# Kernel optimization log

Measured on AMD Instinct MI355X. Metric: run time of the kernel, lower is better.

## Reference

```python
import jax, jax.numpy as jnp
import numpy as np

N_NODES = 50000
N_EDGES = 312500
IN_F = 256
OUT_F = 256


def setup_inputs() -> dict:
    key = jax.random.key(0)
    kx, ki, kj, kw, kb = jax.random.split(key, 5)
    x = jax.random.normal(kx, (N_NODES, IN_F), dtype=jnp.float32)
    Ai = jax.random.randint(ki, (N_EDGES,), 0, N_NODES, dtype=jnp.int64)
    Aj = jax.random.randint(kj, (N_EDGES,), 0, N_NODES, dtype=jnp.int64)
    # Linear(2*in_features, out_features): PyTorch default uniform(-1/sqrt(fan_in), 1/sqrt(fan_in))
    bound = 1.0 / np.sqrt(2 * IN_F)
    W = jax.random.uniform(kw, (OUT_F, 2 * IN_F), dtype=jnp.float32, minval=-bound, maxval=bound)
    b = jax.random.uniform(kb, (OUT_F,), dtype=jnp.float32, minval=-bound, maxval=bound)
    return {"x": x, "W": W, "b": b, "Ai": Ai, "Aj": Aj}


def reference(x, W, b, Ai, Aj):
    X_i = x[Ai]                      # [E, F] gather source rows
    X_j = x[Aj]                      # [E, F]
    X_ij = jnp.concatenate([X_i, X_j], axis=1)   # [E, 2F]
    E_msg = jnp.einsum('ef,of->eo', X_ij, W) + b  # [E, out]
    agg_xi = jax.ops.segment_sum(E_msg, Ai, num_segments=N_NODES)  # [N, out]
    return agg_xi
```

## Files before the change

kernel.cpp:

```cpp
#include <hip/hip_runtime.h>
#include <hip/hip_bf16.h>

#define NN 50000
#define NE 312500
#define FIN 256
#define NT 1564
#define CAP 64

typedef __attribute__((ext_vector_type(4))) float f32x4;
typedef __attribute__((ext_vector_type(2))) float f32x2;
typedef __attribute__((ext_vector_type(8))) short bf16x8;
typedef __attribute__((ext_vector_type(4))) unsigned short u16x4;
typedef __attribute__((ext_vector_type(8))) unsigned short u16x8;
typedef __attribute__((ext_vector_type(4))) unsigned int u32x4;

#ifndef __has_builtin
#define __has_builtin(x) 0
#endif
#if __has_builtin(__builtin_amdgcn_cvt_pk_f32_fp8) && __has_builtin(__builtin_amdgcn_cvt_pk_fp8_f32)
#define HWFP8 1
#else
#define HWFP8 0
#endif

__device__ __forceinline__ float bf2f(unsigned short u) {
  return __builtin_bit_cast(float, ((unsigned int)u) << 16);
}
__device__ __forceinline__ unsigned short f2bf(float f) {
  return __builtin_bit_cast(unsigned short, __float2bfloat16(f));
}

#if !HWFP8
__device__ __forceinline__ unsigned enc8(float f) {
  unsigned bits = __builtin_bit_cast(unsigned, f);
  unsigned s = bits >> 31;
  unsigned a = bits & 0x7FFFFFFFu;
  if (a < 0x3C400000u) return s << 7;
  a += 0x0007FFFFu + ((a >> 20) & 1);
  unsigned e = (a >> 23) - 120u;
  unsigned m = (a >> 20) & 7u;
  if (e > 15u) { e = 15u; m = 6u; }
  return (s << 7) | (e << 3) | m;
}
__device__ __forceinline__ float dec8(unsigned b) {
  unsigned s = (b >> 7) & 1u, e = (b >> 3) & 15u, m = b & 7u;
  float v = e ? __builtin_bit_cast(float, ((e + 120u) << 23) | (m << 20))
              : (float)m * 0.001953125f;
  return s ? -v : v;
}
#endif

__device__ __forceinline__ unsigned enc4fp8(float a, float b, float c, float d) {
#if HWFP8
  int pk = __builtin_amdgcn_cvt_pk_fp8_f32(a, b, 0, false);
  pk = __builtin_amdgcn_cvt_pk_fp8_f32(c, d, pk, true);
  return (unsigned)pk;
#else
  return enc8(a) | (enc8(b) << 8) | (enc8(c) << 16) | (enc8(d) << 24);
#endif
}

__device__ __forceinline__ void dec4fp8(unsigned w, float* r) {
#if HWFP8
  f32x2 lo = __builtin_amdgcn_cvt_pk_f32_fp8((int)w, false);
  f32x2 hi = __builtin_amdgcn_cvt_pk_f32_fp8((int)w, true);
  r[0] = lo[0]; r[1] = lo[1]; r[2] = hi[0]; r[3] = hi[1];
#else
  r[0] = dec8(w & 255); r[1] = dec8((w >> 8) & 255);
  r[2] = dec8((w >> 16) & 255); r[3] = dec8(w >> 24);
#endif
}

__device__ __forceinline__ bf16x8 cvt8v(f32x4 a, f32x4 b) {
  bf16x8 r;
  #pragma unroll
  for (int i = 0; i < 4; ++i) {
    r[i]     = (short)f2bf(a[i]);
    r[i + 4] = (short)f2bf(b[i]);
  }
  return r;
}

__device__ __forceinline__ bf16x8 cvt8(const float* p) {
  return cvt8v(*(const f32x4*)p, *(const f32x4*)(p + 4));
}

__global__ __launch_bounds__(256) void k_wz(const float* __restrict__ W,
                                            unsigned short* __restrict__ WbP,
                                            int* __restrict__ deg) {
  if (blockIdx.x >= 64) {
    int i = (blockIdx.x - 64) * 256 + threadIdx.x;
    if (i < 50048) deg[i] = 0;
    return;
  }
  int lane = threadIdx.x & 63, wid = threadIdx.x >> 6;
  int c = blockIdx.x * 4 + wid;
  int o16 = c >> 3, kk = c & 7;
  int lr = lane & 15, lk = lane >> 4;
  int o = o16 * 16 + lr;
  int k = kk * 32 + lk * 8;
  const float* src = (o < 256) ? (W + (size_t)o * 512 + k)
                               : (W + (size_t)(o - 256) * 512 + 256 + k);
  *(bf16x8*)(WbP + (size_t)c * 512 + lane * 8) = cvt8(src);
}

__global__ __launch_bounds__(512) void k_gemm(
    const float* __restrict__ x, const unsigned short* __restrict__ WbP,
    unsigned short* __restrict__ Y1b, unsigned char* __restrict__ Y2f8,
    const int* __restrict__ Ai, const int* __restrict__ Aj,
    int* __restrict__ deg, int* __restrict__ edst) {
  __shared__ __align__(16) unsigned short A[2][8192];
  const int tid = threadIdx.x;
  const int lane = tid & 63, w = tid >> 6;
  const int lr = lane & 15, lk = lane >> 4;

  for (int e = blockIdx.x * 512 + tid; e < NE; e += 256 * 512) {
    int a = Ai[e];
    int p = atomicAdd(&deg[a], 1);
    edst[a * CAP + p] = Aj[e];
  }

  bf16x8 B[8][4];
  #pragma unroll
  for (int kk = 0; kk < 8; ++kk)
    #pragma unroll
    for (int n = 0; n < 4; ++n)
      B[kk][n] = *(const bf16x8*)(WbP + ((size_t)(w * 4 + n) * 8 + kk) * 512 + lane * 8);
  #pragma unroll
  for (int kk = 0; kk < 8; ++kk)
    #pragma unroll
    for (int n = 0; n < 4; ++n)
      asm volatile("" : "+v"(B[kk][n]));

  const int row0 = (tid >> 5);
  const int seg = tid & 31;
  const int uoff0 = ((row0 >> 4) * 8 + (seg >> 2)) * 512 +
                    (((((seg & 3) * 16) + (row0 & 15)) * 8) ^ ((seg & 7) << 3));
  const int row1 = 16 + row0;
  const int uoff1 = ((row1 >> 4) * 8 + (seg >> 2)) * 512 +
                    (((((seg & 3) * 16) + (row1 & 15)) * 8) ^ ((seg & 7) << 3));

  int tile = blockIdx.x;
  {
    int g0 = tile * 32 + row0; if (g0 > NN - 1) g0 = NN - 1;
    int g1 = tile * 32 + row1; if (g1 > NN - 1) g1 = NN - 1;
    const float* s0 = x + (size_t)g0 * FIN + seg * 8;
    const float* s1 = x + (size_t)g1 * FIN + seg * 8;
    f32x4 a0 = *(const f32x4*)s0, b0 = *(const f32x4*)(s0 + 4);
    f32x4 a1 = *(const f32x4*)s1, b1 = *(const f32x4*)(s1 + 4);
    *(bf16x8*)(&A[0][uoff0]) = cvt8v(a0, b0);
    *(bf16x8*)(&A[0][uoff1]) = cvt8v(a1, b1);
  }
  __syncthreads();

  int p = 0;
  for (; tile < NT; tile += 256) {
    const int nxt = tile + 256;
    const bool hn = (nxt < NT);

    f32x4 a0, b0, a1, b1;
    if (hn) {
      int g0 = nxt * 32 + row0; if (g0 > NN - 1) g0 = NN - 1;
      int g1 = nxt * 32 + row1; if (g1 > NN - 1) g1 = NN - 1;
      const float* s0 = x + (size_t)g0 * FIN + seg * 8;
      const float* s1 = x + (size_t)g1 * FIN + seg * 8;
      a0 = *(const f32x4*)s0; b0 = *(const f32x4*)(s0 + 4);
      a1 = *(const f32x4*)s1; b1 = *(const f32x4*)(s1 + 4);
    }

    f32x4 acc[2][4];
    #pragma unroll
    for (int rg = 0; rg < 2; ++rg)
      #pragma unroll
      for (int n = 0; n < 4; ++n) acc[rg][n] = (f32x4){0.f, 0.f, 0.f, 0.f};
    #pragma unroll
    for (int rg = 0; rg < 2; ++rg) {
      #pragma unroll
      for (int kk = 0; kk < 8; ++kk) {
        bf16x8 af = *(const bf16x8*)(
            &A[p][(rg * 8 + kk) * 512 + ((lane * 8) ^ (((kk & 1) << 5) | (lk << 3)))]);
        #pragma unroll
        for (int n = 0; n < 4; ++n)
          acc[rg][n] = __builtin_amdgcn_mfma_f32_16x16x32_bf16(af, B[kk][n], acc[rg][n], 0, 0, 0);
      }
    }

    #pragma unroll
    for (int rg = 0; rg < 2; ++rg) {
      #pragma unroll
      for (int rr = 0; rr < 4; ++rr) {
        int row = tile * 32 + rg * 16 + lk * 4 + rr;
        if (w < 4) {
          u16x4 v;
          #pragma unroll
          for (int n = 0; n < 4; ++n)
            v[n] = f2bf(acc[rg][n][rr]);
          *(u16x4*)(Y1b + (size_t)row * 256 + w * 64 + lr * 4) = v;
        } else {
          unsigned pk = enc4fp8(acc[rg][0][rr], acc[rg][1][rr],
                                acc[rg][2][rr], acc[rg][3][rr]);
          *(unsigned int*)(Y2f8 + (size_t)row * 256 + (w - 4) * 64 + lr * 4) = pk;
        }
      }
    }

    if (hn) {
      *(bf16x8*)(&A[p ^ 1][uoff0]) = cvt8v(a0, b0);
      *(bf16x8*)(&A[p ^ 1][uoff1]) = cvt8v(a1, b1);
      __syncthreads();
    }
    p ^= 1;
  }
}

__global__ __launch_bounds__(256) void k_epi(
    const unsigned short* __restrict__ Y1b, const unsigned char* __restrict__ Y2f8,
    const int* __restrict__ deg, const int* __restrict__ edst,
    const float* __restrict__ bias, float* __restrict__ out) {
  __shared__ float sm[2048];
  int wid = threadIdx.x >> 6;
  int lane = threadIdx.x & 63;
  int half = lane >> 5;
  int es = (lane >> 4) & 1;
  int fg = lane & 15;
  int base = blockIdx.x * 8 + wid * 2;
  int n = base + half;
  int o = n * CAP;
  int c = deg[n];

  u16x8 y10 = *(const u16x8*)(Y1b + (size_t)n * 256 + fg * 16);
  u16x8 y11 = *(const u16x8*)(Y1b + (size_t)n * 256 + fg * 16 + 8);

  const unsigned char* Y2 = Y2f8 + fg * 16;
  f32x4 ac[4];
  #pragma unroll
  for (int h = 0; h < 4; ++h) ac[h] = (f32x4){0.f, 0.f, 0.f, 0.f};

  int e = es;
  for (; e + 2 < c; e += 4) {
    int jA = edst[o + e];
    int jB = edst[o + e + 2];
    u32x4 vA = *(const u32x4*)(Y2 + (size_t)jA * 256);
    u32x4 vB = *(const u32x4*)(Y2 + (size_t)jB * 256);
    #pragma unroll
    for (int h = 0; h < 4; ++h) {
      float rA[4], rB[4];
      dec4fp8(vA[h], rA);
      dec4fp8(vB[h], rB);
      #pragma unroll
      for (int i = 0; i < 4; ++i) ac[h][i] += rA[i] + rB[i];
    }
  }
  if (e < c) {
    int j = edst[o + e];
    u32x4 v = *(const u32x4*)(Y2 + (size_t)j * 256);
    #pragma unroll
    for (int h = 0; h < 4; ++h) {
      float r[4];
      dec4fp8(v[h], r);
      #pragma unroll
      for (int i = 0; i < 4; ++i) ac[h][i] += r[i];
    }
  }

  #pragma unroll
  for (int h = 0; h < 4; ++h)
    #pragma unroll
    for (int i = 0; i < 4; ++i)
      ac[h][i] += __shfl_xor(ac[h][i], 16);

  float* Wm = sm + (wid * 2 + half) * 256;
  if (es == 0) {
    float dg = (float)c;
    #pragma unroll
    for (int i = 0; i < 16; ++i) {
      int p = fg * 16 + i;
      int tc = (p & ~63) | ((p & 3) << 4) | ((p >> 2) & 15);
      float y1 = bf2f((i < 8) ? y10[i] : y11[i - 8]);
      Wm[tc] = dg * (y1 + bias[tc]) + ac[i >> 2][i & 3];
    }
  }
  asm volatile("s_waitcnt lgkmcnt(0)" ::: "memory");
  #pragma unroll
  for (int h = 0; h < 2; ++h) {
    f32x4 res = *(const f32x4*)(sm + (wid * 2 + h) * 256 + lane * 4);
    __builtin_nontemporal_store(res, (f32x4*)out + (size_t)(base + h) * 64 + lane);
  }
}

extern "C" void kernel_launch(void* const* d_in, const int* in_sizes, int n_in,
                              void* d_out, int out_size, void* d_ws, size_t ws_size,
                              hipStream_t stream) {
  const float* x = (const float*)d_in[0];
  const float* W = (const float*)d_in[1];
  const float* b = (const float*)d_in[2];
  const int* Ai = (const int*)d_in[3];
  const int* Aj = (const int*)d_in[4];
  float* out = (float*)d_out;

  int* ip = (int*)d_ws;
  int* deg  = ip;
  int* edst = ip + 50048;
  unsigned short* WbP  = (unsigned short*)(ip + 3253120);
  unsigned short* Y1b  = (unsigned short*)(ip + 3318656);
  unsigned char*  Y2f8 = (unsigned char*)(ip + 9724800);

  k_wz<<<260, 256, 0, stream>>>(W, WbP, deg);
  k_gemm<<<256, 512, 0, stream>>>(x, WbP, Y1b, Y2f8, Ai, Aj, deg, edst);
  k_epi<<<6250, 256, 0, stream>>>(Y1b, Y2f8, deg, edst, b, out);
}
```

Baseline: 69.45 us.

## Deepen x-tile prefetch to two tiles with triple-buffered LDS and overlap edge binning

Issues global loads for the first two x tiles before the edge-binning atomic loop, so the loads overlap with the atomics. The GEMM loop switches from double to triple LDS buffering with register ping-pong staging, prefetching two tiles ahead. It also writes the next tile into LDS before the MFMA work rather than after. This uses more LDS and registers, and replaces __syncthreads with a manual waitcnt plus barrier, which may lower occupancy or risk subtle sync bugs.

```diff
diff --git a/kernel.cpp b/kernel.cpp
--- a/kernel.cpp
+++ b/kernel.cpp
@@ -109,28 +109,17 @@
     unsigned short* __restrict__ Y1b, unsigned char* __restrict__ Y2f8,
     const int* __restrict__ Ai, const int* __restrict__ Aj,
     int* __restrict__ deg, int* __restrict__ edst) {
-  __shared__ __align__(16) unsigned short A[2][8192];
+  __shared__ __align__(16) unsigned short A[3][8192];
   const int tid = threadIdx.x;
   const int lane = tid & 63, w = tid >> 6;
   const int lr = lane & 15, lk = lane >> 4;
 
-  for (int e = blockIdx.x * 512 + tid; e < NE; e += 256 * 512) {
-    int a = Ai[e];
-    int p = atomicAdd(&deg[a], 1);
-    edst[a * CAP + p] = Aj[e];
-  }
-
   bf16x8 B[8][4];
   #pragma unroll
   for (int kk = 0; kk < 8; ++kk)
     #pragma unroll
     for (int n = 0; n < 4; ++n)
       B[kk][n] = *(const bf16x8*)(WbP + ((size_t)(w * 4 + n) * 8 + kk) * 512 + lane * 8);
-  #pragma unroll
-  for (int kk = 0; kk < 8; ++kk)
-    #pragma unroll
-    for (int n = 0; n < 4; ++n)
-      asm volatile("" : "+v"(B[kk][n]));
 
   const int row0 = (tid >> 5);
   const int seg = tid & 31;
@@ -139,33 +128,73 @@
   const int row1 = 16 + row0;
   const int uoff1 = ((row1 >> 4) * 8 + (seg >> 2)) * 512 +
                     (((((seg & 3) * 16) + (row1 & 15)) * 8) ^ ((seg & 7) << 3));
-
-  int tile = blockIdx.x;
+  const int t0 = blockIdx.x;
+
+  f32x4 s0a, s0b, s0c, s0d, s1a, s1b, s1c, s1d;
   {
-    int g0 = tile * 32 + row0; if (g0 > NN - 1) g0 = NN - 1;
-    int g1 = tile * 32 + row1; if (g1 > NN - 1) g1 = NN - 1;
-    const float* s0 = x + (size_t)g0 * FIN + seg * 8;
-    const float* s1 = x + (size_t)g1 * FIN + seg * 8;
-    f32x4 a0 = *(const f32x4*)s0, b0 = *(const f32x4*)(s0 + 4);
-    f32x4 a1 = *(const f32x4*)s1, b1 = *(const f32x4*)(s1 + 4);
-    *(bf16x8*)(&A[0][uoff0]) = cvt8v(a0, b0);
-    *(bf16x8*)(&A[0][uoff1]) = cvt8v(a1, b1);
-  }
-  __syncthreads();
-
-  int p = 0;
-  for (; tile < NT; tile += 256) {
+    int g0 = t0 * 32 + row0; if (g0 > NN - 1) g0 = NN - 1;
+    int g1 = t0 * 32 + row1; if (g1 > NN - 1) g1 = NN - 1;
+    const float* p0 = x + (size_t)g0 * FIN + seg * 8;
+    const float* p1 = x + (size_t)g1 * FIN + seg * 8;
+    s0a = *(const f32x4*)p0; s0b = *(const f32x4*)(p0 + 4);
+    s0c = *(const f32x4*)p1; s0d = *(const f32x4*)(p1 + 4);
+    int t1 = t0 + 256;
+    int h0 = t1 * 32 + row0; if (h0 > NN - 1) h0 = NN - 1;
+    int h1 = t1 * 32 + row1; if (h1 > NN - 1) h1 = NN - 1;
+    const float* q0 = x + (size_t)h0 * FIN + seg * 8;
+    const float* q1 = x + (size_t)h1 * FIN + seg * 8;
+    s1a = *(const f32x4*)q0; s1b = *(const f32x4*)(q0 + 4);
+    s1c = *(const f32x4*)q1; s1d = *(const f32x4*)(q1 + 4);
+  }
+
+  for (int e = blockIdx.x * 512 + tid; e < NE; e += 256 * 512) {
+    int a = Ai[e];
+    int p = atomicAdd(&deg[a], 1);
+    edst[a * CAP + p] = Aj[e];
+  }
+
+  #pragma unroll
+  for (int kk = 0; kk < 8; ++kk)
+    #pragma unroll
+    for (int n = 0; n < 4; ++n)
+      asm volatile("" : "+v"(B[kk][n]));
+
+  *(bf16x8*)(&A[0][uoff0]) = cvt8v(s0a, s0b);
+  *(bf16x8*)(&A[0][uoff1]) = cvt8v(s0c, s0d);
+  asm volatile("s_waitcnt lgkmcnt(0)" ::: "memory");
+  __builtin_amdgcn_s_barrier();
+
+  int it = 0;
+  for (int tile = t0; tile < NT; tile += 256, ++it) {
+    const int buf = it % 3;
+    const int nbf = (it + 1) % 3;
     const int nxt = tile + 256;
-    const bool hn = (nxt < NT);
-
-    f32x4 a0, b0, a1, b1;
-    if (hn) {
-      int g0 = nxt * 32 + row0; if (g0 > NN - 1) g0 = NN - 1;
-      int g1 = nxt * 32 + row1; if (g1 > NN - 1) g1 = NN - 1;
-      const float* s0 = x + (size_t)g0 * FIN + seg * 8;
-      const float* s1 = x + (size_t)g1 * FIN + seg * 8;
-      a0 = *(const f32x4*)s0; b0 = *(const f32x4*)(s0 + 4);
-      a1 = *(const f32x4*)s1; b1 = *(const f32x4*)(s1 + 4);
+    const int nx2 = tile + 512;
+    const bool h1 = (nxt < NT);
+    const bool h2 = (nx2 < NT);
+    const bool par = (it & 1);
+
+    if (h1) {
+      if (!par) {
+        *(bf16x8*)(&A[nbf][uoff0]) = cvt8v(s1a, s1b);
+        *(bf16x8*)(&A[nbf][uoff1]) = cvt8v(s1c, s1d);
+      } else {
+        *(bf16x8*)(&A[nbf][uoff0]) = cvt8v(s0a, s0b);
+        *(bf16x8*)(&A[nbf][uoff1]) = cvt8v(s0c, s0d);
+      }
+    }
+    if (h2) {
+      int g0 = nx2 * 32 + row0; if (g0 > NN - 1) g0 = NN - 1;
+      int g1 = nx2 * 32 + row1; if (g1 > NN - 1) g1 = NN - 1;
+      const float* p0 = x + (size_t)g0 * FIN + seg * 8;
+      const float* p1 = x + (size_t)g1 * FIN + seg * 8;
+      if (!par) {
+        s0a = *(const f32x4*)p0; s0b = *(const f32x4*)(p0 + 4);
+        s0c = *(const f32x4*)p1; s0d = *(const f32x4*)(p1 + 4);
+      } else {
+        s1a = *(const f32x4*)p0; s1b = *(const f32x4*)(p0 + 4);
+        s1c = *(const f32x4*)p1; s1d = *(const f32x4*)(p1 + 4);
+      }
     }
 
     f32x4 acc[2][4];
@@ -178,7 +207,7 @@
       #pragma unroll
       for (int kk = 0; kk < 8; ++kk) {
         bf16x8 af = *(const bf16x8*)(
-            &A[p][(rg * 8 + kk) * 512 + ((lane * 8) ^ (((kk & 1) << 5) | (lk << 3)))]);
+            &A[buf][(rg * 8 + kk) * 512 + ((lane * 8) ^ (((kk & 1) << 5) | (lk << 3)))]);
         #pragma unroll
         for (int n = 0; n < 4; ++n)
           acc[rg][n] = __builtin_amdgcn_mfma_f32_16x16x32_bf16(af, B[kk][n], acc[rg][n], 0, 0, 0);
@@ -204,12 +233,10 @@
       }
     }
 
-    if (hn) {
-      *(bf16x8*)(&A[p ^ 1][uoff0]) = cvt8v(a0, b0);
-      *(bf16x8*)(&A[p ^ 1][uoff1]) = cvt8v(a1, b1);
-      __syncthreads();
-    }
-    p ^= 1;
+    if (h1) {
+      asm volatile("s_waitcnt lgkmcnt(0)" ::: "memory");
+      __builtin_amdgcn_s_barrier();
+    }
   }
 }
 
```

Result: slower. 72.18 us (+3.9%).
